# Optimization experiments

Measured on AMD Instinct MI355X. Metric: run time of the kernel, lower is better.

The kernel has to match this reference:

```python
import jax, jax.numpy as jnp
import numpy as np

B, S, D_IN, H, NH, L = 8, 1024, 512, 1024, 16, 4
HD = H // NH
SCALE = HD ** -0.5
EPS = 1e-5


def _ln(x, g, b):
    m = jnp.mean(x, axis=-1, keepdims=True)
    v = jnp.mean((x - m) ** 2, axis=-1, keepdims=True)
    return (x - m) * jax.lax.rsqrt(v + EPS) * g + b


def setup_inputs() -> dict:
    key = jax.random.key(0)
    ks = jax.random.split(key, 12)
    s = lambda k, shape, fan: jax.random.normal(k, shape, jnp.float32) * (fan ** -0.5)
    return {
        "x": jax.random.normal(ks[0], (B, S, D_IN), jnp.float32),
        "W_in": s(ks[1], (D_IN, H), D_IN), "b_in": jnp.zeros((H,), jnp.float32),
        "W_qkv": s(ks[2], (L, H, 3 * H), H), "b_qkv": jnp.zeros((L, 3 * H), jnp.float32),
        "W_o": s(ks[3], (L, H, H), H), "b_o": jnp.zeros((L, H), jnp.float32),
        "g1": jnp.ones((L, H), jnp.float32), "be1": jnp.zeros((L, H), jnp.float32),
        "W_out": s(ks[4], (H, H), H), "b_out": jnp.zeros((H,), jnp.float32),
        "g2": jnp.ones((H,), jnp.float32), "be2": jnp.zeros((H,), jnp.float32),
    }


def _attn_layer(x, Wqkv, bqkv, Wo, bo, g, be):
    b, s, h = x.shape
    qkv = (x @ Wqkv + bqkv).reshape(b, s, 3, NH, HD)
    q = qkv[:, :, 0].transpose(0, 2, 1, 3)  # [B,NH,S,HD]
    k = qkv[:, :, 1].transpose(0, 2, 1, 3)
    v = qkv[:, :, 2].transpose(0, 2, 1, 3)
    scores = jnp.einsum("bhqd,bhkd->bhqk", q, k) * SCALE
    w = jax.nn.softmax(scores, axis=-1)  # dropout is identity in eval
    o = jnp.einsum("bhqk,bhkd->bhqd", w, v)
    o = o.transpose(0, 2, 1, 3).reshape(b, s, h)
    return _ln(o @ Wo + bo + x, g, be)


def reference(x, W_in, b_in, W_qkv, b_qkv, W_o, b_o, g1, be1, W_out, b_out, g2, be2):
    h = x @ W_in + b_in
    for i in range(L):
        h = _attn_layer(h, W_qkv[i], b_qkv[i], W_o[i], b_o[i], g1[i], be1[i])
    pooled = jnp.mean(h, axis=1)  # [B,H]
    return _ln(pooled @ W_out + b_out, g2, be2)
```

## Files before the change

### kernel.cpp

```cpp
#include <hip/hip_runtime.h>
#include <stdint.h>

typedef unsigned short u16;
typedef unsigned int   u32;
typedef __attribute__((ext_vector_type(8))) short short8;
typedef __attribute__((ext_vector_type(4))) float f32x4;
typedef __attribute__((ext_vector_type(16))) float f32x16;
typedef __attribute__((ext_vector_type(2))) unsigned int uint2v;

#define B_   8
#define S_   1024
#define DIN_ 512
#define H_   1024
#define NH_  16
#define HD_  64
#define L_   4
#define M_   (B_*S_)
#define SCALE_ 0.125f
#define EPS_ 1e-5f

__device__ __forceinline__ u16 f2b(float f) {
  u32 u = __builtin_bit_cast(u32, f);
  u32 r = (u + 0x7fffu + ((u >> 16) & 1u)) >> 16;
  return (u16)r;
}

__device__ __forceinline__ u32 cvtpk(float lo, float hi) {
  u32 r;
  asm("v_cvt_pk_bf16_f32 %0, %1, %2" : "=v"(r) : "v"(lo), "v"(hi));
  return r;
}

__device__ __forceinline__ void gll16(const void* g, void* l) {
  __builtin_amdgcn_global_load_lds(
      (const __attribute__((address_space(1))) u32*)(uintptr_t)g,
      (__attribute__((address_space(3))) u32*)(uintptr_t)l,
      16, 0, 0);
}

__global__ void cvt_k(const float* __restrict__ in, u16* __restrict__ out) {
  long i = (long)(blockIdx.x * 256 + threadIdx.x) * 4;
  f32x4 v = *(const f32x4*)&in[i];
  u32 p0 = (u32)f2b(v[0]) | ((u32)f2b(v[1]) << 16);
  u32 p1 = (u32)f2b(v[2]) | ((u32)f2b(v[3]) << 16);
  u32* o = (u32*)&out[i];
  o[0] = p0; o[1] = p1;
}

__global__ __launch_bounds__(256)
void tcvt_k(const float* __restrict__ in0, u16* __restrict__ out0, int R, int C) {
  __shared__ float t[32][33];
  const float* in = in0 + (size_t)blockIdx.z * R * C;
  u16* out = out0 + (size_t)blockIdx.z * R * C;
  int tx = threadIdx.x & 31, ty = threadIdx.x >> 5;
  long r0 = blockIdx.y * 32, c0 = blockIdx.x * 32;
#pragma unroll
  for (int i = 0; i < 4; ++i)
    t[ty + i*8][tx] = in[(r0 + ty + i*8) * (long)C + c0 + tx];
  __syncthreads();
#pragma unroll
  for (int i = 0; i < 4; ++i)
    out[(c0 + ty + i*8) * (long)R + r0 + tx] = f2b(t[tx][ty + i*8]);
}

template<int EPI>
__global__ __launch_bounds__(256, 2)
void gemm_k(const u16* __restrict__ A, const u16* __restrict__ Bt,
            const float* __restrict__ bias,
            float* __restrict__ Cf, u16* __restrict__ Cb,
            const float* __restrict__ Res,
            int Ndim, int K, int scale_cols)
{
  __shared__ u16 As[128 * 32];
  __shared__ u16 Bs[128 * 32];
  const int tid = threadIdx.x;
  const int lane = tid & 63;
  const int wid = tid >> 6;
  const int wr = wid >> 1, wc = wid & 1;
  const int l15 = lane & 15, l4 = lane >> 4;
  const long arow0 = (long)blockIdx.x * 128;
  const long brow0 = (long)blockIdx.y * 128;

  f32x4 acc[4][4] = {};

  const int srow = tid >> 2;
  const int scol = (tid & 3) * 8;
  const u16* ga  = A  + (arow0 + srow) * K + scol;
  const u16* ga1 = ga + 64 * (long)K;
  const u16* gb  = Bt + (brow0 + srow) * K + scol;
  const u16* gb1 = gb + 64 * (long)K;
  u16* lA0 = &As[tid * 8];
  u16* lA1 = &As[2048 + tid * 8];
  u16* lB0 = &Bs[tid * 8];
  u16* lB1 = &Bs[2048 + tid * 8];

  for (int k0 = 0; k0 < K; k0 += 32) {
    gll16(ga + k0, lA0);
    gll16(ga1 + k0, lA1);
    gll16(gb + k0, lB0);
    gll16(gb1 + k0, lB1);
    __syncthreads();
    short8 af[4], bf[4];
#pragma unroll
    for (int m = 0; m < 4; ++m)
      af[m] = *(const short8*)&As[(wr*64 + m*16 + l15) * 32 + l4*8];
#pragma unroll
    for (int n = 0; n < 4; ++n)
      bf[n] = *(const short8*)&Bs[(wc*64 + n*16 + l15) * 32 + l4*8];
#pragma unroll
    for (int m = 0; m < 4; ++m)
#pragma unroll
      for (int n = 0; n < 4; ++n)
        acc[m][n] = __builtin_amdgcn_mfma_f32_16x16x32_bf16(af[m], bf[n], acc[m][n], 0, 0, 0);
    __syncthreads();
  }

  const int crow = wr*64 + l4*4;
  const int ccol = wc*64 + l15;
#pragma unroll
  for (int m = 0; m < 4; ++m) {
#pragma unroll
    for (int n = 0; n < 4; ++n) {
      const int col = (int)brow0 + ccol + n*16;
      const float bv = bias[col];
      const float sc = (EPI == 1 && col < scale_cols) ? SCALE_ : 1.0f;
#pragma unroll
      for (int r = 0; r < 4; ++r) {
        const long row = arow0 + crow + m*16 + r;
        float v = acc[m][n][r] + bv;
        if (EPI == 1) {
          Cb[row * Ndim + col] = f2b(v * sc);
        } else if (EPI == 0) {
          Cf[row * Ndim + col] = v;
          Cb[row * Ndim + col] = f2b(v);
        } else {
          Cf[row * Ndim + col] = v + Res[row * Ndim + col];
        }
      }
    }
  }
}

__global__ __launch_bounds__(512, 1)
void gemm8_k(const u16* __restrict__ A, const u16* __restrict__ Bt,
             const float* __restrict__ bias, u16* __restrict__ Cb)
{
  constexpr int K = 1024, N = 3 * H_;
  constexpr int NT = K / 64;
  __shared__ u16 lds[8][8192];

  const int tid = threadIdx.x;
  const int lane = tid & 63;
  const int wid = tid >> 6;
  const int wm = wid >> 2, wn = wid & 3;
  const int l15 = lane & 15, l4 = lane >> 4;

  const int bid = blockIdx.x;
  const int xcd = bid & 7, idx = bid >> 3;
  const long arow0 = (long)(xcd * 4 + (idx & 3)) * 256;
  const long brow0 = (long)(idx >> 2) * 256;

  f32x4 acc[8][4] = {};
  short8 bfr[4][2];
  short8 afr[2][2];

  auto stage = [&](int buf, int op, int half, int kt) {
    const u16* src = op ? Bt : A;
    const long rb = (op ? brow0 : arow0) + half * 128;
    u16* dst = lds[buf*4 + op*2 + half];
#pragma unroll
    for (int ld = 0; ld < 2; ++ld) {
      int p = ld * 512 + tid;
      int row = p >> 3;
      int kc = (p & 7) ^ (row & 7);
      gll16(src + (rb + row) * (long)K + kt * 64 + kc * 8, (char*)dst + p * 16);
    }
  };
  auto readB = [&](int buf) {
    const char* base = (const char*)lds[buf*4 + 2 + (wn >> 1)];
#pragma unroll
    for (int n = 0; n < 4; ++n)
#pragma unroll
      for (int ks = 0; ks < 2; ++ks) {
        int rh = (wn & 1) * 64 + n * 16 + l15;
        int byt = rh * 128 + ((((ks*4 + l4) * 16)) ^ ((rh & 7) << 4));
        bfr[n][ks] = *(const short8*)(base + byt);
      }
  };
  auto readA = [&](int buf, int q) {
    const char* base = (const char*)lds[buf*4 + wm];
#pragma unroll
    for (int j = 0; j < 2; ++j)
#pragma unroll
      for (int ks = 0; ks < 2; ++ks) {
        int rh = (2*q + j) * 16 + l15;
        int byt = rh * 128 + ((((ks*4 + l4) * 16)) ^ ((rh & 7) << 4));
        afr[j][ks] = *(const short8*)(base + byt);
      }
  };
  auto mm = [&](int q) {
    __builtin_amdgcn_s_setprio(1);
#pragma unroll
    for (int j = 0; j < 2; ++j)
#pragma unroll
      for (int n = 0; n < 4; ++n)
#pragma unroll
        for (int ks = 0; ks < 2; ++ks)
          acc[2*q+j][n] = __builtin_amdgcn_mfma_f32_16x16x32_bf16(
              afr[j][ks], bfr[n][ks], acc[2*q+j][n], 0, 0, 0);
    __builtin_amdgcn_s_setprio(0);
  };

#define PH(cb, q, doB, sb, so, sh, st, doV)                       \
    readA(cb, q); if (doB) readB(cb);                             \
    stage(sb, so, sh, st);                                        \
    __builtin_amdgcn_s_barrier();                                 \
    mm(q);                                                        \
    if (doV) asm volatile("s_waitcnt vmcnt(6)" ::: "memory");     \
    __builtin_amdgcn_s_barrier();

  stage(0,1,0,0); stage(0,1,1,0); stage(0,0,0,0); stage(0,0,1,0);
  stage(1,1,0,1); stage(1,1,1,1); stage(1,0,0,1);
  asm volatile("s_waitcnt vmcnt(6)" ::: "memory");
  __builtin_amdgcn_s_barrier();

  const int niter = NT / 2;
  for (int i = 0; i < niter; ++i) {
    const int tO  = 2*i + 1;
    const int tE2 = (2*i + 2 < NT) ? 2*i + 2 : NT - 1;
    const int tO2 = (2*i + 3 < NT) ? 2*i + 3 : NT - 1;
    PH(0, 0, true , 1, 0, 1, tO , false)
    PH(0, 1, false, 0, 1, 0, tE2, false)
    PH(0, 2, false, 0, 1, 1, tE2, false)
    PH(0, 3, false, 0, 0, 0, tE2, true )
    PH(1, 0, true , 0, 0, 1, tE2, false)
    PH(1, 1, false, 1, 1, 0, tO2, false)
    PH(1, 2, false, 1, 1, 1, tO2, false)
    PH(1, 3, false, 1, 0, 0, tO2, true )
  }
#undef PH

  const long crow0 = arow0 + wm * 128;
  const int  ccol0 = (int)brow0 + wn * 64;
#pragma unroll
  for (int m = 0; m < 8; ++m) {
#pragma unroll
    for (int n = 0; n < 4; ++n) {
      const int col = ccol0 + n * 16 + l15;
      const float bv = bias[col];
      const float sc = (col < H_) ? SCALE_ : 1.0f;
#pragma unroll
      for (int r = 0; r < 4; ++r) {
        const long row = crow0 + m * 16 + l4 * 4 + r;
        Cb[row * N + col] = f2b((acc[m][n][r] + bv) * sc);
      }
    }
  }
}

__global__ __launch_bounds__(512)
void attn_k(const u16* __restrict__ qkv, u16* __restrict__ ob)
{
  __shared__ u16 Ks[2][4096];
  __shared__ u16 Vs[2][4096];

  const int tid = threadIdx.x, lane = tid & 63, wid = tid >> 6;
  const int l31 = lane & 31, hi = lane >> 5;

  const int blk = blockIdx.x;
  const int xcd = blk & 7, slot = blk >> 3;
  const int bh = xcd + ((slot >> 2) << 3);
  const int qx = slot & 3;
  const int b = bh >> 4, nh = bh & 15;
  const int q0 = qx * 256 + wid * 32;

  const int RS = 3 * H_;
  const long base = (long)b * S_ * RS;
  const u16* Qg = qkv + base + nh * HD_;
  const u16* Kg = qkv + base + H_ + nh * HD_;
  const u16* Vg = qkv + base + 2 * H_ + nh * HD_;

  short8 qf[4];
#pragma unroll
  for (int ks = 0; ks < 4; ++ks)
    qf[ks] = *(const short8*)&Qg[(long)(q0 + l31) * RS + ks*16 + hi*8];

  float m_ = -1e30f, l_ = 0.f;
  f32x16 o0 = {}, o1 = {};

  const int krow = tid >> 3, kc = tid & 7;
  const int ksc = kc ^ (krow & 7);
  const long kgoff = (long)krow * RS + ksc * 8;
  const int vd = tid & 63, vch = tid >> 6;
  const int vbyt = (vd*128 + vch*16) ^ ((vd & 7) << 4);

  {
    gll16(Kg + kgoff, (char*)&Ks[0][0] + tid*16);
    union { u16 u[8]; short8 v; } tv;
#pragma unroll
    for (int j = 0; j < 8; ++j)
      tv.u[j] = Vg[(long)(vch*8 + j) * RS + vd];
    *(short8*)((char*)&Vs[0][0] + vbyt) = tv.v;
  }
  __syncthreads();

  for (int t = 0; t < 16; ++t) {
    const int cur = t & 1, nxt = cur ^ 1;
    union { u16 u[8]; short8 v; } ta;
    if (t < 15) {
      const long kv1 = (long)(t + 1) * 64;
      gll16(Kg + kv1 * RS + kgoff, (char*)&Ks[nxt][0] + tid*16);
#pragma unroll
      for (int j = 0; j < 8; ++j)
        ta.u[j] = Vg[(kv1 + vch*8 + j) * RS + vd];
    }

    f32x16 s0 = {}, s1 = {};
    __builtin_amdgcn_s_setprio(1);
#pragma unroll
    for (int ks = 0; ks < 4; ++ks) {
      const int koff = ks*32 + hi*16;
      const int by0 = (l31*128 + koff) ^ ((l31 & 7) << 4);
      short8 kf0 = *(const short8*)((const char*)&Ks[cur][0] + by0);
      s0 = __builtin_amdgcn_mfma_f32_32x32x16_bf16(kf0, qf[ks], s0, 0, 0, 0);
      const int by1 = ((32 + l31)*128 + koff) ^ ((l31 & 7) << 4);
      short8 kf1 = *(const short8*)((const char*)&Ks[cur][0] + by1);
      s1 = __builtin_amdgcn_mfma_f32_32x32x16_bf16(kf1, qf[ks], s1, 0, 0, 0);
    }
    __builtin_amdgcn_s_setprio(0);

    float tmax = -1e30f;
#pragma unroll
    for (int r = 0; r < 16; ++r) tmax = fmaxf(tmax, fmaxf(s0[r], s1[r]));
    tmax = fmaxf(tmax, __shfl_xor(tmax, 32));
    if (!__all(tmax <= m_ + 8.f)) {
      const float mnew = fmaxf(m_, tmax);
      const float corr = __expf(m_ - mnew);
      m_ = mnew; l_ *= corr;
#pragma unroll
      for (int r = 0; r < 16; ++r) {
        float cr = __shfl(corr, (r&3) + 8*(r>>2) + 4*hi);
        o0[r] *= cr; o1[r] *= cr;
      }
    }
    float sum = 0.f;
#pragma unroll
    for (int r = 0; r < 16; ++r) {
      float p0 = __expf(s0[r] - m_);
      float p1 = __expf(s1[r] - m_);
      s0[r] = p0; s1[r] = p1;
      sum += p0 + p1;
    }
    sum += __shfl_xor(sum, 32);
    l_ += sum;

    short8 pa[4];
#pragma unroll
    for (int ks2 = 0; ks2 < 2; ++ks2) {
      const int r0 = 8 * ks2;
      u32 A0 = cvtpk(s0[r0+0], s0[r0+1]), A1 = cvtpk(s0[r0+2], s0[r0+3]);
      u32 B0 = cvtpk(s0[r0+4], s0[r0+5]), B1 = cvtpk(s0[r0+6], s0[r0+7]);
      uint2v w02 = __builtin_amdgcn_permlane32_swap(A0, B0, false, false);
      uint2v w13 = __builtin_amdgcn_permlane32_swap(A1, B1, false, false);
      union { u32 w[4]; short8 v; } u_;
      u_.w[0] = w02.x; u_.w[1] = w13.x; u_.w[2] = w02.y; u_.w[3] = w13.y;
      pa[ks2] = u_.v;
    }
#pragma unroll
    for (int ks2 = 0; ks2 < 2; ++ks2) {
      const int r0 = 8 * ks2;
      u32 A0 = cvtpk(s1[r0+0], s1[r0+1]), A1 = cvtpk(s1[r0+2], s1[r0+3]);
      u32 B0 = cvtpk(s1[r0+4], s1[r0+5]), B1 = cvtpk(s1[r0+6], s1[r0+7]);
      uint2v w02 = __builtin_amdgcn_permlane32_swap(A0, B0, false, false);
      uint2v w13 = __builtin_amdgcn_permlane32_swap(A1, B1, false, false);
      union { u32 w[4]; short8 v; } u_;
      u_.w[0] = w02.x; u_.w[1] = w13.x; u_.w[2] = w02.y; u_.w[3] = w13.y;
      pa[2 + ks2] = u_.v;
    }

    __builtin_amdgcn_s_setprio(1);
#pragma unroll
    for (int ks = 0; ks < 4; ++ks) {
      const int vb = ks*32 + hi*16;
      const int by0 = (l31*128 + vb) ^ ((l31 & 7) << 4);
      short8 v0 = *(const short8*)((const char*)&Vs[cur][0] + by0);
      o0 = __builtin_amdgcn_mfma_f32_32x32x16_bf16(pa[ks], v0, o0, 0, 0, 0);
      const int by1 = ((32 + l31)*128 + vb) ^ ((l31 & 7) << 4);
      short8 v1 = *(const short8*)((const char*)&Vs[cur][0] + by1);
      o1 = __builtin_amdgcn_mfma_f32_32x32x16_bf16(pa[ks], v1, o1, 0, 0, 0);
    }
    __builtin_amdgcn_s_setprio(0);

    if (t < 15) {
      *(short8*)((char*)&Vs[nxt][0] + vbyt) = ta.v;
      __syncthreads();
    }
  }

  const float linv = 1.0f / l_;
#pragma unroll
  for (int r = 0; r < 16; ++r) {
    const int rowq = (r&3) + 8*(r>>2) + 4*hi;
    const float li = __shfl(linv, rowq);
    const long srow = (long)(b * S_ + q0 + rowq);
    ob[srow * H_ + nh*HD_ + l31]      = f2b(o0[r] * li);
    ob[srow * H_ + nh*HD_ + 32 + l31] = f2b(o1[r] * li);
  }
}

__global__ __launch_bounds__(256)
void ln_k(const float* __restrict__ in, const float* __restrict__ g,
          const float* __restrict__ be, float* __restrict__ outf,
          u16* __restrict__ outb, const float* __restrict__ bias)
{
  const int row = blockIdx.x;
  const int tid = threadIdx.x;
  const float* x = in + (long)row * H_;
  f32x4 v = *(const f32x4*)&x[tid * 4];
  if (bias) {
    f32x4 bv = *(const f32x4*)&bias[tid * 4];
    v[0] += bv[0]; v[1] += bv[1]; v[2] += bv[2]; v[3] += bv[3];
  }
  float s  = v[0] + v[1] + v[2] + v[3];
  float ss = v[0]*v[0] + v[1]*v[1] + v[2]*v[2] + v[3]*v[3];
#pragma unroll
  for (int o = 1; o < 64; o <<= 1) {
    s  += __shfl_xor(s, o);
    ss += __shfl_xor(ss, o);
  }
  __shared__ float rs[4], rq[4];
  const int wid = tid >> 6;
  if ((tid & 63) == 0) { rs[wid] = s; rq[wid] = ss; }
  __syncthreads();
  float ts = rs[0] + rs[1] + rs[2] + rs[3];
  float tq = rq[0] + rq[1] + rq[2] + rq[3];
  const float mu = ts * (1.0f / H_);
  const float var = tq * (1.0f / H_) - mu * mu;
  const float rstd = rsqrtf(var + EPS_);
  const long obase = (long)row * H_ + tid * 4;
#pragma unroll
  for (int j = 0; j < 4; ++j) {
    int c = tid * 4 + j;
    float y = (v[j] - mu) * rstd * g[c] + be[c];
    outf[obase + j] = y;
    if (outb) outb[obase + j] = f2b(y);
  }
}

__global__ void pool_k(const float* __restrict__ hf, float* __restrict__ pooled) {
  const int c = blockIdx.x * 256 + threadIdx.x;
  const int b = blockIdx.y;
  const int s0 = blockIdx.z * 128;
  float s = 0.f;
  for (int t = 0; t < 128; ++t) s += hf[((long)(b * S_ + s0 + t)) * H_ + c];
  atomicAdd(&pooled[b * H_ + c], s * (1.0f / S_));
}

__global__ void fgemm_k(const float* __restrict__ pooled, const float* __restrict__ W,
                        float* __restrict__ out) {
  const int n = blockIdx.x * 64 + threadIdx.x;
  const int b = blockIdx.y;
  const int k0 = blockIdx.z * 128;
  const float* pr = pooled + b * H_ + k0;
  const float* wr = W + (long)k0 * H_ + n;
  float s = 0.f;
#pragma unroll 8
  for (int k = 0; k < 128; ++k)
    s += pr[k] * wr[(long)k * H_];
  atomicAdd(&out[b * H_ + n], s);
}

extern "C" void kernel_launch(void* const* d_in, const int* in_sizes, int n_in,
                              void* d_out, int out_size, void* d_ws, size_t ws_size,
                              hipStream_t stream) {
  const float* x     = (const float*)d_in[0];
  const float* W_in  = (const float*)d_in[1];
  const float* b_in  = (const float*)d_in[2];
  const float* W_qkv = (const float*)d_in[3];
  const float* b_qkv = (const float*)d_in[4];
  const float* W_o   = (const float*)d_in[5];
  const float* b_o   = (const float*)d_in[6];
  const float* g1    = (const float*)d_in[7];
  const float* be1   = (const float*)d_in[8];
  const float* W_out = (const float*)d_in[9];
  const float* b_out = (const float*)d_in[10];
  const float* g2    = (const float*)d_in[11];
  const float* be2   = (const float*)d_in[12];
  float* outp = (float*)d_out;

  char* ws = (char*)d_ws;
  float* hf    = (float*)(ws + 0);
  u16*   hb    = (u16*)(ws + 33554432);
  u16*   qkvb  = (u16*)(ws + 50331648);
  float* resf  = (float*)(ws + 50331648);
  u16*   ob    = (u16*)(ws + 100663296);
  u16*   xb    = (u16*)(ws + 100663296);
  u16*   WinT  = (u16*)(ws + 117440512);
  u16*   WqkvT = (u16*)(ws + 118489088);
  u16*   WoT   = (u16*)(ws + 143654912);
  float* pooled= (float*)(ws + 152043520);
  float* tmpf  = (float*)(ws + 152076288);

  cvt_k<<<dim3(M_ * DIN_ / 1024), 256, 0, stream>>>(x, xb);
  tcvt_k<<<dim3(H_/32, DIN_/32, 1), 256, 0, stream>>>(W_in, WinT, DIN_, H_);
  tcvt_k<<<dim3(3*H_/32, H_/32, L_), 256, 0, stream>>>(W_qkv, WqkvT, H_, 3*H_);
  tcvt_k<<<dim3(H_/32, H_/32, L_), 256, 0, stream>>>(W_o, WoT, H_, H_);

  gemm_k<0><<<dim3(M_/128, H_/128), 256, 0, stream>>>(xb, WinT, b_in, hf, hb, nullptr, H_, DIN_, 0);

  for (int l = 0; l < L_; ++l) {
    gemm8_k<<<dim3((M_/256) * (3*H_/256)), 512, 0, stream>>>(hb, WqkvT + (size_t)l*3*H_*H_,
                                                             b_qkv + l*3*H_, qkvb);
    attn_k<<<dim3(512), 512, 0, stream>>>(qkvb, ob);
    gemm_k<2><<<dim3(M_/128, H_/128), 256, 0, stream>>>(ob, WoT + (size_t)l*H_*H_,
                                                        b_o + l*H_, resf, nullptr, hf,
                                                        H_, H_, 0);
    ln_k<<<dim3(M_), 256, 0, stream>>>(resf, g1 + l*H_, be1 + l*H_, hf, hb, nullptr);
  }

  hipMemsetAsync(pooled, 0, B_ * H_ * sizeof(float), stream);
  hipMemsetAsync(tmpf, 0, B_ * H_ * sizeof(float), stream);
  pool_k<<<dim3(H_/256, B_, 8), 256, 0, stream>>>(hf, pooled);
  fgemm_k<<<dim3(H_/64, B_, 8), 64, 0, stream>>>(pooled, W_out, tmpf);
  ln_k<<<dim3(B_), 256, 0, stream>>>(tmpf, g2, be2, outp, nullptr, b_out);
}
```

Before: 882.0 us.

## Halve attention block size, fold log2e into Q scale, use exp2

The attention kernel now runs 1024 blocks of 256 threads, each covering 128 queries, instead of 512 blocks of 512 threads. Each thread loads two K/V chunks per tile to fill shared memory. Q is pre-scaled by log2(e) in the QKV GEMM epilogue, so the softmax can use the native exp2 instruction, and the lazy-rescale threshold is scaled to match. The row max and sum now use tree reductions to shorten dependency chains. The aim is more resident blocks and cheaper exponentials, at the cost of twice the K/V loads per query and more load work per thread.

```diff
diff --git a/kernel.cpp b/kernel.cpp
--- a/kernel.cpp
+++ b/kernel.cpp
@@ -17,6 +17,7 @@
 #define L_   4
 #define M_   (B_*S_)
 #define SCALE_ 0.125f
+#define LOG2E_ 1.44269504088896f
 #define EPS_ 1e-5f
 
 __device__ __forceinline__ u16 f2b(float f) {
@@ -248,7 +249,7 @@
     for (int n = 0; n < 4; ++n) {
       const int col = ccol0 + n * 16 + l15;
       const float bv = bias[col];
-      const float sc = (col < H_) ? SCALE_ : 1.0f;
+      const float sc = (col < H_) ? (SCALE_ * LOG2E_) : 1.0f;
 #pragma unroll
       for (int r = 0; r < 4; ++r) {
         const long row = crow0 + m * 16 + l4 * 4 + r;
@@ -258,7 +259,7 @@
   }
 }
 
-__global__ __launch_bounds__(512)
+__global__ __launch_bounds__(256)
 void attn_k(const u16* __restrict__ qkv, u16* __restrict__ ob)
 {
   __shared__ u16 Ks[2][4096];
@@ -269,10 +270,10 @@
 
   const int blk = blockIdx.x;
   const int xcd = blk & 7, slot = blk >> 3;
-  const int bh = xcd + ((slot >> 2) << 3);
-  const int qx = slot & 3;
+  const int bh = xcd + ((slot >> 3) << 3);
+  const int qx = slot & 7;
   const int b = bh >> 4, nh = bh & 15;
-  const int q0 = qx * 256 + wid * 32;
+  const int q0 = qx * 128 + wid * 32;
 
   const int RS = 3 * H_;
   const long base = (long)b * S_ * RS;
@@ -288,31 +289,40 @@
   float m_ = -1e30f, l_ = 0.f;
   f32x16 o0 = {}, o1 = {};
 
-  const int krow = tid >> 3, kc = tid & 7;
-  const int ksc = kc ^ (krow & 7);
-  const long kgoff = (long)krow * RS + ksc * 8;
+  const int kr0 = tid >> 3, kc0 = (tid & 7) ^ (kr0 & 7);
+  const int kr1 = (256 + tid) >> 3, kc1 = (tid & 7) ^ (kr1 & 7);
+  const long kg0 = (long)kr0 * RS + kc0 * 8;
+  const long kg1 = (long)kr1 * RS + kc1 * 8;
   const int vd = tid & 63, vch = tid >> 6;
-  const int vbyt = (vd*128 + vch*16) ^ ((vd & 7) << 4);
+  const int vbyt0 = (vd*128 + vch*16) ^ ((vd & 7) << 4);
+  const int vbyt1 = (vd*128 + 64 + vch*16) ^ ((vd & 7) << 4);
 
   {
-    gll16(Kg + kgoff, (char*)&Ks[0][0] + tid*16);
-    union { u16 u[8]; short8 v; } tv;
-#pragma unroll
-    for (int j = 0; j < 8; ++j)
-      tv.u[j] = Vg[(long)(vch*8 + j) * RS + vd];
-    *(short8*)((char*)&Vs[0][0] + vbyt) = tv.v;
+    gll16(Kg + kg0, (char*)&Ks[0][0] + tid*16);
+    gll16(Kg + kg1, (char*)&Ks[0][0] + (256 + tid)*16);
+    union { u16 u[8]; short8 v; } ta, tb;
+#pragma unroll
+    for (int j = 0; j < 8; ++j) {
+      ta.u[j] = Vg[(long)(vch*8 + j) * RS + vd];
+      tb.u[j] = Vg[(long)(32 + vch*8 + j) * RS + vd];
+    }
+    *(short8*)((char*)&Vs[0][0] + vbyt0) = ta.v;
+    *(short8*)((char*)&Vs[0][0] + vbyt1) = tb.v;
   }
   __syncthreads();
 
   for (int t = 0; t < 16; ++t) {
     const int cur = t & 1, nxt = cur ^ 1;
-    union { u16 u[8]; short8 v; } ta;
+    union { u16 u[8]; short8 v; } ta, tb;
     if (t < 15) {
       const long kv1 = (long)(t + 1) * 64;
-      gll16(Kg + kv1 * RS + kgoff, (char*)&Ks[nxt][0] + tid*16);
-#pragma unroll
-      for (int j = 0; j < 8; ++j)
+      gll16(Kg + kv1 * RS + kg0, (char*)&Ks[nxt][0] + tid*16);
+      gll16(Kg + kv1 * RS + kg1, (char*)&Ks[nxt][0] + (256 + tid)*16);
+#pragma unroll
+      for (int j = 0; j < 8; ++j) {
         ta.u[j] = Vg[(kv1 + vch*8 + j) * RS + vd];
+        tb.u[j] = Vg[(kv1 + 32 + vch*8 + j) * RS + vd];
+      }
     }
 
     f32x16 s0 = {}, s1 = {};
@@ -329,13 +339,17 @@
     }
     __builtin_amdgcn_s_setprio(0);
 
-    float tmax = -1e30f;
-#pragma unroll
-    for (int r = 0; r < 16; ++r) tmax = fmaxf(tmax, fmaxf(s0[r], s1[r]));
-    tmax = fmaxf(tmax, __shfl_xor(tmax, 32));
-    if (!__all(tmax <= m_ + 8.f)) {
+    float t16[16];
+#pragma unroll
+    for (int r = 0; r < 16; ++r) t16[r] = fmaxf(s0[r], s1[r]);
+#pragma unroll
+    for (int st = 8; st > 0; st >>= 1)
+#pragma unroll
+      for (int r = 0; r < st; ++r) t16[r] = fmaxf(t16[r], t16[r + st]);
+    float tmax = fmaxf(t16[0], __shfl_xor(t16[0], 32));
+    if (!__all(tmax <= m_ + 11.54f)) {
       const float mnew = fmaxf(m_, tmax);
-      const float corr = __expf(m_ - mnew);
+      const float corr = __builtin_amdgcn_exp2f(m_ - mnew);
       m_ = mnew; l_ *= corr;
 #pragma unroll
       for (int r = 0; r < 16; ++r) {
@@ -343,14 +357,22 @@
         o0[r] *= cr; o1[r] *= cr;
       }
     }
-    float sum = 0.f;
-#pragma unroll
-    for (int r = 0; r < 16; ++r) {
-      float p0 = __expf(s0[r] - m_);
-      float p1 = __expf(s1[r] - m_);
-      s0[r] = p0; s1[r] = p1;
-      sum += p0 + p1;
-    }
+    float a0 = 0.f, a1 = 0.f, a2 = 0.f, a3 = 0.f;
+#pragma unroll
+    for (int r = 0; r < 16; r += 4) {
+      float p00 = __builtin_amdgcn_exp2f(s0[r+0] - m_);
+      float p01 = __builtin_amdgcn_exp2f(s0[r+1] - m_);
+      float p02 = __builtin_amdgcn_exp2f(s0[r+2] - m_);
+      float p03 = __builtin_amdgcn_exp2f(s0[r+3] - m_);
+      float p10 = __builtin_amdgcn_exp2f(s1[r+0] - m_);
+      float p11 = __builtin_amdgcn_exp2f(s1[r+1] - m_);
+      float p12 = __builtin_amdgcn_exp2f(s1[r+2] - m_);
+      float p13 = __builtin_amdgcn_exp2f(s1[r+3] - m_);
+      s0[r+0] = p00; s0[r+1] = p01; s0[r+2] = p02; s0[r+3] = p03;
+      s1[r+0] = p10; s1[r+1] = p11; s1[r+2] = p12; s1[r+3] = p13;
+      a0 += p00 + p10; a1 += p01 + p11; a2 += p02 + p12; a3 += p03 + p13;
+    }
+    float sum = (a0 + a1) + (a2 + a3);
     sum += __shfl_xor(sum, 32);
     l_ += sum;
 
@@ -392,7 +414,8 @@
     __builtin_amdgcn_s_setprio(0);
 
     if (t < 15) {
-      *(short8*)((char*)&Vs[nxt][0] + vbyt) = ta.v;
+      *(short8*)((char*)&Vs[nxt][0] + vbyt0) = ta.v;
+      *(short8*)((char*)&Vs[nxt][0] + vbyt1) = tb.v;
       __syncthreads();
     }
   }
@@ -511,7 +534,7 @@
   for (int l = 0; l < L_; ++l) {
     gemm8_k<<<dim3((M_/256) * (3*H_/256)), 512, 0, stream>>>(hb, WqkvT + (size_t)l*3*H_*H_,
                                                              b_qkv + l*3*H_, qkvb);
-    attn_k<<<dim3(512), 512, 0, stream>>>(qkvb, ob);
+    attn_k<<<dim3(1024), 256, 0, stream>>>(qkvb, ob);
     gemm_k<2><<<dim3(M_/128, H_/128), 256, 0, stream>>>(ob, WoT + (size_t)l*H_*H_,
                                                         b_o + l*H_, resf, nullptr, hf,
                                                         H_, H_, 0);
```

New measurement: 905.4 us. 1.03x slower.
